# Kernel optimization log

Measured on AMD Instinct MI355X. Metric: run time of the kernel, lower is better.

## Reference

```python
import jax, jax.numpy as jnp
import numpy as np

B, N, M, DIM, H, DH = 2, 1024, 32, 128, 8, 16
DI = H * DH          # dim_inner = 128
S = 5                # sum of (1, max_degree, max_degree), max_degree = 2
DMLP = 256           # int(2.0 * dim_inner)
EPS = 1e-5
CLAMP = 50.0

def _ln(x, w):
    mu = x.mean(-1, keepdims=True)
    var = ((x - mu) ** 2).mean(-1, keepdims=True)
    return (x - mu) / jnp.sqrt(var + EPS) * w

def _split_heads(t):
    t = t.reshape(*t.shape[:-1], H, DH)
    return jnp.moveaxis(t, -2, 1)

def _gather(t, idx):
    # t: (b, h, n, ...), idx: (b, n, m) -> (b, h, n, m, ...)
    return jax.vmap(lambda tb, ib: tb[:, ib])(t, idx)

def setup_inputs():
    key = jax.random.key(0)
    ks = jax.random.split(key, 30)
    nrm = lambda i, shp, s=1.0: jax.random.normal(ks[i], shp, jnp.float32) * s
    return dict(
        h=nrm(0, (B, N, DIM)),
        t_ij=nrm(1, (B, N, M, DIM)),
        r_ij_1=nrm(2, (B, N, M, 3)),
        r_ij_2=nrm(3, (B, N, M, 5)),
        x_1=nrm(4, (B, N, DIM, 3)),
        x_2=nrm(5, (B, N, DIM, 5)),
        neighbor_indices=jax.random.randint(ks[6], (B, N, M), 0, N),
        neighbor_mask=jnp.ones((B, N, M), dtype=bool),
        ln_i_w=jnp.ones((DIM,)),
        ln_j_w=jnp.ones((DIM,)),
        Wq=nrm(7, (DIM, DI), DIM ** -0.5),
        Wk=nrm(8, (DIM, DI), DIM ** -0.5),
        Wv1=nrm(9, (DIM, DMLP), DIM ** -0.5), bv1=jnp.zeros((DMLP,)),
        Wv2=nrm(10, (DMLP, S * DI), DMLP ** -0.5), bv2=jnp.zeros((S * DI,)),
        Wpv1=nrm(11, (DIM, DMLP), DIM ** -0.5), bpv1=jnp.zeros((DMLP,)),
        Wpv2=nrm(12, (DMLP, S * DI), DMLP ** -0.5), bpv2=jnp.zeros((S * DI,)),
        Wek=nrm(13, (DIM, S * DI), DIM ** -0.5),
        Wev=nrm(14, (DIM, S * DI), DIM ** -0.5),
        Wg=nrm(15, (DIM, H * S), DIM ** -0.5), bg=jnp.zeros((H * S,)),
        Wo=nrm(16, (DI, DIM), DI ** -0.5),
    )

def reference(h, t_ij, r_ij_1, r_ij_2, x_1, x_2, neighbor_indices, neighbor_mask,
              ln_i_w, ln_j_w, Wq, Wk, Wv1, bv1, Wv2, bv2, Wpv1, bpv1, Wpv2, bpv2,
              Wek, Wev, Wg, bg, Wo):
    hi = _ln(h, ln_i_w)
    hj = _ln(h, ln_j_w)
    q = _split_heads(hi @ Wq)                                                   # (b,h,n,dh)
    k = _split_heads(hj @ Wk)                                                   # (b,h,n,dh)
    v = _split_heads((jax.nn.silu(hj @ Wv1 + bv1) @ Wv2 + bv2).reshape(B, N, S, DI))       # (b,h,n,s,dh)
    pv = _split_heads((jax.nn.silu(hj @ Wpv1 + bpv1) @ Wpv2 + bpv2).reshape(B, N, S, DI))  # (b,h,n,s,dh)
    ek = _split_heads(jax.nn.silu(t_ij @ Wek).reshape(B, N, M, S, DI))          # (b,h,i,j,s,dh)
    ev = _split_heads((t_ij @ Wev).reshape(B, N, M, S, DI))                     # (b,h,i,j,s,dh)

    idx = neighbor_indices
    k_n = _gather(k, idx)                                                        # (b,h,i,j,dh)
    v_n = _gather(v, idx)                                                        # (b,h,i,j,s,dh)
    pv_n = _gather(pv, idx)                                                      # (b,h,i,j,s,dh)

    keys = k_n[..., None, :] * ek                                                # (b,h,i,j,s,dh)
    sim = jnp.einsum('bhid,bhijsd->bhijs', q, keys)
    sim = jnp.tanh(sim / CLAMP) * CLAMP
    neg = -jnp.finfo(sim.dtype).max
    sim = jnp.where(neighbor_mask[:, None, :, :, None], sim, neg)
    attn = jax.nn.softmax(sim, axis=-2)                                          # softmax over neighbors j

    sea = attn[..., None] * v_n + ev * pv_n                                      # (b,h,i,j,s,dh)
    gates = jax.nn.sigmoid(hi @ Wg + bg).reshape(B, N, H, S)
    gates = jnp.moveaxis(gates, 2, 1)[:, :, :, None, :, None]                    # (b,h,i,1,s,1)
    out = sea * gates
    out = jnp.moveaxis(out, 1, -2).reshape(B, N, M, S, DI)                       # merge heads
    out = out @ Wo                                                               # (b,i,j,s,dim)

    h_res = out[:, :, :, 0, :].sum(axis=2)                                       # (b,i,dim)
    r_sc1, r_sc2 = out[:, :, :, 1, :], out[:, :, :, 2, :]
    x_sc1, x_sc2 = out[:, :, :, 3, :], out[:, :, :, 4, :]

    def deg_residual(r_ij_l, x_l, r_sc, x_sc):
        r_res = jnp.einsum('bijm,bijd->bidm', r_ij_l, r_sc)
        x_nbr = jax.vmap(lambda xb, ib: xb[ib])(x_l, idx)                        # (b,i,j,d,m)
        x_res = jnp.einsum('bijdm,bijd->bidm', x_nbr, x_sc)
        return r_res + x_res

    x_res_1 = deg_residual(r_ij_1, x_1, r_sc1, x_sc1)
    x_res_2 = deg_residual(r_ij_2, x_2, r_sc2, x_sc2)
    return (h_res, x_res_1, x_res_2)
```

## Files before the change

kernel.cpp:

```cpp
#include <hip/hip_runtime.h>
#include <hip/hip_bf16.h>
#include <math.h>

#define BB    2
#define NPTS  1024
#define MM    32
#define DIMM  128
#define HH    8
#define DHH   16
#define SS    5
#define DMLPC 256
#define SDI   640
#define NNODE (BB*NPTS)
#define NN128 (NNODE*DIMM)

typedef __attribute__((ext_vector_type(8))) short bf16x8;
typedef __attribute__((ext_vector_type(4))) float f32x4;
typedef __attribute__((ext_vector_type(4))) float fvec4;

__device__ __forceinline__ float frcp(float x){ return __builtin_amdgcn_rcpf(x); }
__device__ __forceinline__ float sigf(float x){ return frcp(1.0f+__expf(-x)); }
__device__ __forceinline__ float siluf(float x){ return x*frcp(1.0f+__expf(-x)); }
__device__ __forceinline__ unsigned short f2bf(float x){
  unsigned u = __float_as_uint(x);
  u += 0x7fffu + ((u>>16)&1u);
  return (unsigned short)(u>>16);
}
__device__ __forceinline__ float bfu2f(unsigned short u){ return __uint_as_float(((unsigned)u)<<16); }

#define SWZT 76544
#define T4C  2097152
__global__ __launch_bounds__(256) void prep_kernel(
    const float* __restrict__ Wq,  const float* __restrict__ Wk,
    const float* __restrict__ Wv1, const float* __restrict__ Wpv1,
    const float* __restrict__ Wv2, const float* __restrict__ Wpv2,
    const float* __restrict__ Wek, const float* __restrict__ Wev,
    const float* __restrict__ Wo,  const float* __restrict__ Wg,
    const float* __restrict__ t_ij, const float* __restrict__ x1g,
    const float* __restrict__ x2g,
    unsigned short* __restrict__ wsw, unsigned short* __restrict__ tb,
    unsigned short* __restrict__ x1p, unsigned short* __restrict__ x2p)
{
  int i = blockIdx.x*256 + threadIdx.x;
  if (i < SWZT){
    int f = i >> 6, lane = i & 63;
    const float* W; int ncols, nkt, fb;
    if      (f <   32){ W=Wq;   ncols=128; nkt=4; fb=0;    }
    else if (f <   64){ W=Wk;   ncols=128; nkt=4; fb=32;   }
    else if (f <  128){ W=Wv1;  ncols=256; nkt=4; fb=64;   }
    else if (f <  192){ W=Wpv1; ncols=256; nkt=4; fb=128;  }
    else if (f <  512){ W=Wv2;  ncols=640; nkt=8; fb=192;  }
    else if (f <  832){ W=Wpv2; ncols=640; nkt=8; fb=512;  }
    else if (f <  992){ W=Wek;  ncols=640; nkt=4; fb=832;  }
    else if (f < 1152){ W=Wev;  ncols=640; nkt=4; fb=992;  }
    else if (f < 1184){ W=Wo;   ncols=128; nkt=4; fb=1152; }
    else              { W=Wg;   ncols=40;  nkt=4; fb=1184; }
    int fl = f - fb;
    int kt = fl % nkt, nt = fl / nkt;
    int row = kt*32 + ((lane>>4)*8);
    int col = nt*16 + (lane&15);
    unsigned px[4];
    if (col < ncols){
      #pragma unroll
      for (int e2=0; e2<4; ++e2){
        unsigned lo = f2bf(W[(size_t)(row+2*e2  )*ncols + col]);
        unsigned hi = f2bf(W[(size_t)(row+2*e2+1)*ncols + col]);
        px[e2] = lo | (hi<<16);
      }
    } else {
      px[0]=px[1]=px[2]=px[3]=0u;
    }
    ((uint4*)wsw)[(size_t)f*64 + lane] = make_uint4(px[0],px[1],px[2],px[3]);
  } else if (i < SWZT + T4C){
    int q = i - SWZT;
    fvec4 v = __builtin_nontemporal_load((const fvec4*)t_ij + q);
    unsigned a = (unsigned)f2bf(v[0]) | ((unsigned)f2bf(v[1])<<16);
    unsigned b = (unsigned)f2bf(v[2]) | ((unsigned)f2bf(v[3])<<16);
    unsigned long long pv = (unsigned long long)a | ((unsigned long long)b << 32);
    __builtin_nontemporal_store(pv, (unsigned long long*)tb + q);
  } else if (i < SWZT + T4C + NN128){
    int nc = i - (SWZT + T4C);
    const float* sp = x1g + (size_t)nc*3;
    unsigned long long pk = (unsigned long long)f2bf(sp[0])
                          | ((unsigned long long)f2bf(sp[1])<<16)
                          | ((unsigned long long)f2bf(sp[2])<<32);
    __builtin_nontemporal_store(pk, (unsigned long long*)(x1p + (size_t)nc*4));
  } else {
    int nc = i - (SWZT + T4C + NN128);
    const float* sp = x2g + (size_t)nc*5;
    unsigned long long lo = (unsigned long long)f2bf(sp[0])
                          | ((unsigned long long)f2bf(sp[1])<<16)
                          | ((unsigned long long)f2bf(sp[2])<<32)
                          | ((unsigned long long)f2bf(sp[3])<<48);
    unsigned long long hi = (unsigned long long)f2bf(sp[4]);
    __builtin_nontemporal_store(lo, (unsigned long long*)(x2p + (size_t)nc*8));
    __builtin_nontemporal_store(hi, (unsigned long long*)(x2p + (size_t)nc*8 + 4));
  }
}

__global__ __launch_bounds__(256) void node_kernel(
    const float* __restrict__ h,
    const float* __restrict__ lniw, const float* __restrict__ lnjw,
    const unsigned short* __restrict__ wsw,
    const float* __restrict__ bv1, const float* __restrict__ bpv1,
    const float* __restrict__ bv2, const float* __restrict__ bpv2,
    const float* __restrict__ bg,
    unsigned short* __restrict__ qb, unsigned short* __restrict__ kb,
    unsigned short* __restrict__ vpvb, float* __restrict__ go)
{
  const int br  = blockIdx.x & 1;
  const int n0  = (blockIdx.x >> 1) * 16;
  const int tid = threadIdx.x;
  const int wid = tid>>6, lane = tid&63;
  const int u   = lane&15;

  const unsigned short* wqk_sw = wsw + (br ? 16384 : 0);
  const unsigned short* w1_sw  = wsw + (br ? 65536 : 32768);
  const unsigned short* w2_sw  = wsw + (br ? 262144 : 98304);
  const unsigned short* wg_sw  = wsw + 606208;
  const float* b1 = br ? bpv1 : bv1;
  const float* b2 = br ? bpv2 : bv2;

  __shared__ unsigned short hib[16][132], hjb[16][132];
  __shared__ unsigned short m1[16][260];

  {
    const int row = tid>>4, cg = tid&15;
    const float* hp = h + (size_t)(n0+row)*DIMM + cg*8;
    fvec4 p0 = *(const fvec4*)hp;
    fvec4 p1 = *(const fvec4*)(hp+4);
    float x[8] = {p0[0],p0[1],p0[2],p0[3],p1[0],p1[1],p1[2],p1[3]};
    float s1=0.f, s2=0.f;
    #pragma unroll
    for (int e=0;e<8;++e){ s1+=x[e]; s2+=x[e]*x[e]; }
    #pragma unroll
    for (int m=1;m<16;m<<=1){ s1+=__shfl_xor(s1,m); s2+=__shfl_xor(s2,m); }
    const float mu = s1*(1.f/DIMM), ms = s2*(1.f/DIMM);
    const float rstd = rsqrtf(ms-mu*mu+1e-5f);
    #pragma unroll
    for (int e=0;e<8;++e){
      float xn = (x[e]-mu)*rstd;
      int c = cg*8+e;
      hib[row][c] = f2bf(xn*lniw[c]);
      hjb[row][c] = f2bf(xn*lnjw[c]);
    }
  }
  __syncthreads();

  bf16x8 aj[4];
  #pragma unroll
  for (int kt=0;kt<4;++kt) aj[kt] = *(const bf16x8*)&hjb[u][kt*32+(lane>>4)*8];

  {
    bf16x8 afr[4];
    if (br == 0){
      #pragma unroll
      for (int kt=0;kt<4;++kt) afr[kt] = *(const bf16x8*)&hib[u][kt*32+(lane>>4)*8];
    } else {
      #pragma unroll
      for (int kt=0;kt<4;++kt) afr[kt] = aj[kt];
    }
    unsigned short* outb = br ? kb : qb;
    const bf16x8* bfp = (const bf16x8*)wqk_sw;
    for (int i2=0;i2<2;++i2){
      const int nt = wid*2+i2;
      f32x4 acc = {0.f,0.f,0.f,0.f};
      #pragma unroll
      for (int kt=0;kt<4;++kt)
        acc = __builtin_amdgcn_mfma_f32_16x16x32_bf16(afr[kt], bfp[(size_t)(nt*4+kt)*64+lane], acc, 0,0,0);
      #pragma unroll
      for (int r=0;r<4;++r)
        outb[(size_t)(n0+(lane>>4)*4+r)*DIMM + nt*16+u] = f2bf(acc[r]);
    }
  }

  {
    const bf16x8* bfp = (const bf16x8*)w1_sw;
    for (int i2=0;i2<4;++i2){
      const int nt = wid*4+i2;
      f32x4 acc = {0.f,0.f,0.f,0.f};
      #pragma unroll
      for (int kt=0;kt<4;++kt)
        acc = __builtin_amdgcn_mfma_f32_16x16x32_bf16(aj[kt], bfp[(size_t)(nt*4+kt)*64+lane], acc, 0,0,0);
      const float bv = b1[nt*16+u];
      #pragma unroll
      for (int r=0;r<4;++r)
        m1[(lane>>4)*4+r][nt*16+u] = f2bf(siluf(acc[r]+bv));
    }
  }
  __syncthreads();

  {
    bf16x8 am[8];
    #pragma unroll
    for (int kt=0;kt<8;++kt) am[kt] = *(const bf16x8*)&m1[u][kt*32+(lane>>4)*8];
    const bf16x8* bfp = (const bf16x8*)w2_sw;
    for (int i2=0;i2<10;++i2){
      const int nt = wid*10+i2;
      f32x4 acc = {0.f,0.f,0.f,0.f};
      #pragma unroll
      for (int kt=0;kt<8;++kt)
        acc = __builtin_amdgcn_mfma_f32_16x16x32_bf16(am[kt], bfp[(size_t)(nt*8+kt)*64+lane], acc, 0,0,0);
      const int c = nt*16+u, s = c>>7, d = c&127;
      const float bb = b2[c];
      #pragma unroll
      for (int r=0;r<4;++r)
        vpvb[(size_t)(n0+(lane>>4)*4+r)*(SS*256) + s*256 + d*2 + br] = f2bf(acc[r]+bb);
    }
  }

  if (br == 0 && wid == 0){
    bf16x8 ai[4];
    #pragma unroll
    for (int kt=0;kt<4;++kt) ai[kt] = *(const bf16x8*)&hib[u][kt*32+(lane>>4)*8];
    const bf16x8* bfp = (const bf16x8*)wg_sw;
    #pragma unroll
    for (int nt=0;nt<3;++nt){
      f32x4 acc = {0.f,0.f,0.f,0.f};
      #pragma unroll
      for (int kt=0;kt<4;++kt)
        acc = __builtin_amdgcn_mfma_f32_16x16x32_bf16(ai[kt], bfp[(size_t)(nt*4+kt)*64+lane], acc, 0,0,0);
      const int col = nt*16+u;
      if (col < HH*SS){
        const float bb = bg[col];
        #pragma unroll
        for (int r=0;r<4;++r)
          go[(size_t)(n0+(lane>>4)*4+r)*(HH*SS) + col] = sigf(acc[r]+bb);
      }
    }
  }
}

__global__ __launch_bounds__(256) void edge_kernel(
    const unsigned short* __restrict__ tb,
    const float* __restrict__ r1g, const float* __restrict__ r2g,
    const unsigned short* __restrict__ x1p, const unsigned short* __restrict__ x2p,
    const int*  __restrict__ nbr,
    const unsigned short* __restrict__ wsw,
    const unsigned short* __restrict__ qb, const unsigned short* __restrict__ kb,
    const unsigned short* __restrict__ vpvb,
    const float* __restrict__ go,
    float* __restrict__ out,
    float* __restrict__ p1, float* __restrict__ p2,
    float* __restrict__ p3, float* __restrict__ p4,
    int use_atomic)
{
  const int bid = blockIdx.x;
  const int xcd = bid & 7, wslot = bid >> 3;
  const int nid = xcd*256 + (wslot & 255);
  const int s   = wslot >> 8;
  const int b0  = nid >> 10;
  const int tid = threadIdx.x;
  const int wid = tid >> 6, lane = tid & 63;
  const int u   = lane & 15;
  const int g4  = (lane >> 4) * 4;

  const bf16x8* wekf = (const bf16x8*)(wsw + 425984);
  const bf16x8* wevf = (const bf16x8*)(wsw + 507904);
  const bf16x8* wof  = (const bf16x8*)(wsw + 589824);

  __shared__ unsigned short buf_lds[MM][132];
  __shared__ float          sim_s[HH][33];
  __shared__ float          g_s[HH];
  __shared__ float          r_s[MM][5];

  bf16x8 afr[2][4];
  {
    const unsigned short* tp = tb + (size_t)nid*MM*DIMM;
    #pragma unroll
    for (int mt=0; mt<2; ++mt)
      #pragma unroll
      for (int kt=0; kt<4; ++kt)
        afr[mt][kt] = *(const bf16x8*)&tp[(mt*16+u)*DIMM + kt*32 + g4*2];
  }

  #pragma unroll
  for (int it=0; it<4; ++it){
    int e = tid + it*256;
    int j = e>>5, d = (e&31)*4;
    int nj = nbr[nid*MM + j];
    *(uint2*)&buf_lds[j][d] = *(const uint2*)&kb[(unsigned)(b0*NPTS + nj)*DIMM + d];
  }
  int njr[2][4];
  #pragma unroll
  for (int mt=0; mt<2; ++mt)
    #pragma unroll
    for (int r=0; r<4; ++r)
      njr[mt][r] = nbr[nid*MM + mt*16 + g4 + r];
  if (tid < HH) g_s[tid] = go[nid*HH*SS + tid*SS + s];
  if (s == 1){ for (int e=tid; e<MM*3; e+=256) r_s[e/3][e%3] = r1g[(size_t)nid*MM*3 + e]; }
  if (s == 2){ for (int e=tid; e<MM*5; e+=256) r_s[e/5][e%5] = r2g[(size_t)nid*MM*5 + e]; }
  const float ql = bfu2f(qb[(unsigned)nid*DIMM + wid*16 + u]);
  const float qh = bfu2f(qb[(unsigned)nid*DIMM + (wid+4)*16 + u]);
  const unsigned* vpvu = (const unsigned*)vpvb;
  unsigned vp[2][2][4];
  #pragma unroll
  for (int hl=0; hl<2; ++hl){
    const int col = (wid*2+hl)*16 + u;
    #pragma unroll
    for (int mt=0; mt<2; ++mt)
      #pragma unroll
      for (int r=0; r<4; ++r)
        vp[hl][mt][r] = vpvu[(unsigned)(b0*NPTS + njr[mt][r])*(SS*DIMM) + s*DIMM + col];
  }
  __syncthreads();

  #pragma unroll
  for (int i=0; i<2; ++i){
    const int hh = wid + 4*i;
    const int nt = s*8 + hh;
    const float qv = i ? qh : ql;
    f32x4 acc0 = {0.f,0.f,0.f,0.f}, acc1 = {0.f,0.f,0.f,0.f};
    #pragma unroll
    for (int kt=0; kt<4; ++kt){
      bf16x8 bfr = wekf[(size_t)(nt*4+kt)*64 + lane];
      acc0 = __builtin_amdgcn_mfma_f32_16x16x32_bf16(afr[0][kt], bfr, acc0, 0,0,0);
      acc1 = __builtin_amdgcn_mfma_f32_16x16x32_bf16(afr[1][kt], bfr, acc1, 0,0,0);
    }
    #pragma unroll
    for (int mt=0; mt<2; ++mt){
      #pragma unroll
      for (int r=0; r<4; ++r){
        int j = mt*16 + g4 + r;
        float val = (mt==0) ? acc0[r] : acc1[r];
        float p = siluf(val) * qv * bfu2f(buf_lds[j][hh*16 + u]);
        p += __shfl_xor(p,1); p += __shfl_xor(p,2);
        p += __shfl_xor(p,4); p += __shfl_xor(p,8);
        if (u == 0) sim_s[hh][j] = p;
      }
    }
  }
  __syncthreads();

  {
    const int hh = tid >> 5, j = tid & 31;
    float praw = sim_s[hh][j];
    float v = 50.f - 100.f*frcp(__expf(praw*0.04f) + 1.f);
    float e = __expf(v);
    float sum = e;
    #pragma unroll
    for (int m=1; m<32; m<<=1) sum += __shfl_xor(sum,m);
    sim_s[hh][j] = g_s[hh] * e * frcp(sum);
  }
  __syncthreads();

  #pragma unroll
  for (int hl=0; hl<2; ++hl){
    const int hh = wid*2 + hl;
    const int nt = s*8 + hh;
    const int col = hh*16 + u;
    const float gp = g_s[hh];
    f32x4 acc0 = {0.f,0.f,0.f,0.f}, acc1 = {0.f,0.f,0.f,0.f};
    #pragma unroll
    for (int kt=0; kt<4; ++kt){
      bf16x8 bfr = wevf[(size_t)(nt*4+kt)*64 + lane];
      acc0 = __builtin_amdgcn_mfma_f32_16x16x32_bf16(afr[0][kt], bfr, acc0, 0,0,0);
      acc1 = __builtin_amdgcn_mfma_f32_16x16x32_bf16(afr[1][kt], bfr, acc1, 0,0,0);
    }
    #pragma unroll
    for (int mt=0; mt<2; ++mt){
      #pragma unroll
      for (int r=0; r<4; ++r){
        int j = mt*16 + g4 + r;
        float evv = (mt==0) ? acc0[r] : acc1[r];
        unsigned w = vp[hl][mt][r];
        float vn  = bfu2f((unsigned short)(w & 0xffffu));
        float pvn = bfu2f((unsigned short)(w >> 16));
        float sea = sim_s[hh][j]*vn + gp*evv*pvn;
        buf_lds[j][col] = f2bf(sea);
      }
    }
  }
  __syncthreads();

  float hres[2] = {0.f,0.f};
  float xr1[2][3] = {{0.f,0.f,0.f},{0.f,0.f,0.f}};
  float xr2[2][5] = {{0.f,0.f,0.f,0.f,0.f},{0.f,0.f,0.f,0.f,0.f}};
  #pragma unroll
  for (int ntl=0; ntl<2; ++ntl){
    const int col = (wid*2+ntl)*16 + u;
    #pragma unroll
    for (int mt=0; mt<2; ++mt){
      f32x4 acc = {0.f,0.f,0.f,0.f};
      #pragma unroll
      for (int kt=0; kt<4; ++kt){
        bf16x8 a = *(const bf16x8*)&buf_lds[mt*16 + u][kt*32 + g4*2];
        bf16x8 wfr = wof[(size_t)((wid*2+ntl)*4+kt)*64 + lane];
        acc = __builtin_amdgcn_mfma_f32_16x16x32_bf16(a, wfr, acc, 0,0,0);
      }
      #pragma unroll
      for (int r=0; r<4; ++r){
        int j = mt*16 + g4 + r;
        float ov = acc[r];
        if (s == 0){
          hres[ntl] += ov;
        } else if (s == 1){
          #pragma unroll
          for (int m=0;m<3;++m) xr1[ntl][m] += r_s[j][m]*ov;
        } else if (s == 2){
          #pragma unroll
          for (int m=0;m<5;++m) xr2[ntl][m] += r_s[j][m]*ov;
        } else if (s == 3){
          unsigned idx = (unsigned)(b0*NPTS + njr[mt][r])*DIMM + col;
          uint2 w2 = *(const uint2*)&x1p[(size_t)idx*4];
          xr1[ntl][0] += bfu2f((unsigned short)(w2.x & 0xffffu))*ov;
          xr1[ntl][1] += bfu2f((unsigned short)(w2.x >> 16))*ov;
          xr1[ntl][2] += bfu2f((unsigned short)(w2.y & 0xffffu))*ov;
        } else {
          unsigned idx = (unsigned)(b0*NPTS + njr[mt][r])*DIMM + col;
          uint4 w4 = *(const uint4*)&x2p[(size_t)idx*8];
          xr2[ntl][0] += bfu2f((unsigned short)(w4.x & 0xffffu))*ov;
          xr2[ntl][1] += bfu2f((unsigned short)(w4.x >> 16))*ov;
          xr2[ntl][2] += bfu2f((unsigned short)(w4.y & 0xffffu))*ov;
          xr2[ntl][3] += bfu2f((unsigned short)(w4.y >> 16))*ov;
          xr2[ntl][4] += bfu2f((unsigned short)(w4.z & 0xffffu))*ov;
        }
      }
    }
  }

  #pragma unroll
  for (int ntl=0; ntl<2; ++ntl){
    hres[ntl] += __shfl_xor(hres[ntl],16); hres[ntl] += __shfl_xor(hres[ntl],32);
    #pragma unroll
    for (int m=0;m<3;++m){ xr1[ntl][m] += __shfl_xor(xr1[ntl][m],16); xr1[ntl][m] += __shfl_xor(xr1[ntl][m],32); }
    #pragma unroll
    for (int m=0;m<5;++m){ xr2[ntl][m] += __shfl_xor(xr2[ntl][m],16); xr2[ntl][m] += __shfl_xor(xr2[ntl][m],32); }
  }
  if (lane < 16){
    const size_t b1 = (size_t)NNODE*DIMM;
    const size_t b2 = b1 + (size_t)NNODE*DIMM*3;
    #pragma unroll
    for (int ntl=0; ntl<2; ++ntl){
      int col = (wid*2+ntl)*16 + lane;
      size_t nc = (size_t)nid*DIMM + col;
      if (s == 0){
        __builtin_nontemporal_store(hres[ntl], &out[nc]);
      } else if (use_atomic){
        if (s == 1 || s == 3){
          #pragma unroll
          for (int m=0;m<3;++m) atomicAdd(&out[b1 + nc*3 + m], xr1[ntl][m]);
        } else {
          #pragma unroll
          for (int m=0;m<5;++m) atomicAdd(&out[b2 + nc*5 + m], xr2[ntl][m]);
        }
      } else {
        if (s == 1){      for (int m=0;m<3;++m) p1[nc*3+m] = xr1[ntl][m]; }
        else if (s == 2){ for (int m=0;m<5;++m) p2[nc*5+m] = xr2[ntl][m]; }
        else if (s == 3){ for (int m=0;m<3;++m) p3[nc*3+m] = xr1[ntl][m]; }
        else {            for (int m=0;m<5;++m) p4[nc*5+m] = xr2[ntl][m]; }
      }
    }
  }
}

__global__ __launch_bounds__(256) void combine_kernel(
    const float* __restrict__ p1, const float* __restrict__ p2,
    const float* __restrict__ p3, const float* __restrict__ p4,
    float* __restrict__ out)
{
  const int N1 = NNODE*DIMM*3/4;
  int i = blockIdx.x*256 + threadIdx.x;
  if (i < N1){
    fvec4 a = ((const fvec4*)p1)[i];
    fvec4 b = ((const fvec4*)p3)[i];
    ((fvec4*)(out + NNODE*DIMM))[i] = a + b;
  } else {
    int q = i - N1;
    fvec4 a = ((const fvec4*)p2)[q];
    fvec4 b = ((const fvec4*)p4)[q];
    ((fvec4*)(out + NNODE*DIMM*4))[q] = a + b;
  }
}

extern "C" void kernel_launch(void* const* d_in, const int* in_sizes, int n_in,
                              void* d_out, int out_size, void* d_ws, size_t ws_size,
                              hipStream_t stream) {
  const float* h    = (const float*)d_in[0];
  const float* t_ij = (const float*)d_in[1];
  const float* r1g  = (const float*)d_in[2];
  const float* r2g  = (const float*)d_in[3];
  const float* x1g  = (const float*)d_in[4];
  const float* x2g  = (const float*)d_in[5];
  const int*   nbr  = (const int*)d_in[6];
  const float* lniw = (const float*)d_in[8];
  const float* lnjw = (const float*)d_in[9];
  const float* Wq   = (const float*)d_in[10];
  const float* Wk   = (const float*)d_in[11];
  const float* Wv1  = (const float*)d_in[12];
  const float* bv1  = (const float*)d_in[13];
  const float* Wv2  = (const float*)d_in[14];
  const float* bv2  = (const float*)d_in[15];
  const float* Wpv1 = (const float*)d_in[16];
  const float* bpv1 = (const float*)d_in[17];
  const float* Wpv2 = (const float*)d_in[18];
  const float* bpv2 = (const float*)d_in[19];
  const float* Wek  = (const float*)d_in[20];
  const float* Wev  = (const float*)d_in[21];
  const float* Wg   = (const float*)d_in[22];
  const float* bg   = (const float*)d_in[23];
  const float* Wo   = (const float*)d_in[24];

  char* w = (char*)d_ws;
  #define CARVE(ty, name, count) ty* name = (ty*)w; w += (((size_t)(count))*sizeof(ty) + 255) & ~(size_t)255;
  CARVE(unsigned short, qb,   (size_t)NNODE*DIMM)
  CARVE(unsigned short, kb,   (size_t)NNODE*DIMM)
  CARVE(unsigned short, vpvb, (size_t)NNODE*SS*256)
  CARVE(float,          go,   (size_t)NNODE*HH*SS)
  CARVE(unsigned short, x1p,  (size_t)NN128*4)
  CARVE(unsigned short, x2p,  (size_t)NN128*8)
  CARVE(unsigned short, tb,   (size_t)NNODE*MM*DIMM)
  CARVE(unsigned short, wsw,  (size_t)1196*512)
  CARVE(float, p1, (size_t)NN128*3)
  CARVE(float, p2, (size_t)NN128*5)
  CARVE(float, p3, (size_t)NN128*3)
  CARVE(float, p4, (size_t)NN128*5)
  #undef CARVE
  int use_atomic = ((size_t)(w - (char*)d_ws) > ws_size) ? 1 : 0;

  float* outp = (float*)d_out;

  if (use_atomic){
    hipError_t _e = hipMemsetAsync(outp + (size_t)NNODE*DIMM, 0,
                                   (size_t)NNODE*DIMM*8*sizeof(float), stream);
    (void)_e;
  }

  prep_kernel<<<10539, 256, 0, stream>>>(Wq, Wk, Wv1, Wpv1, Wv2, Wpv2,
      Wek, Wev, Wo, Wg, t_ij, x1g, x2g, wsw, tb, x1p, x2p);

  node_kernel<<<NNODE/16*2, 256, 0, stream>>>(h, lniw, lnjw, wsw,
      bv1, bpv1, bv2, bpv2, bg, qb, kb, vpvb, go);

  edge_kernel<<<NNODE*SS, 256, 0, stream>>>(tb, r1g, r2g, x1p, x2p, nbr,
      wsw, qb, kb, vpvb, go, outp, p1, p2, p3, p4, use_atomic);

  if (!use_atomic){
    combine_kernel<<<2048, 256, 0, stream>>>(p1, p2, p3, p4, outp);
  }
}
```

Before: 179.2 us.

## Process all five output slots per node in one edge block and drop combine pass

The edge kernel now launches one block per node and loops over the five output slots internally. It used to launch a separate block per (node, slot). This lets the t_ij MFMA fragments, the gathered k rows, the neighbor indices, the gates and the r_ij values be loaded once and reused across slots. The next slot's v/pv gather is prefetched while the current slot's sea tile is written. Heads are remapped so that each wave owns its own rows of sim_s, which removes two block barriers per slot. Because every block now holds full per-node sums, it writes the outputs directly, and the partial buffers, atomic fallback and combine kernel are removed. The trade-off is a five times smaller grid with longer, more serial blocks, which gives fewer resident blocks to hide gather latency.

```diff
diff --git a/kernel.cpp b/kernel.cpp
--- a/kernel.cpp
+++ b/kernel.cpp
@@ -240,15 +240,10 @@
     const unsigned short* __restrict__ qb, const unsigned short* __restrict__ kb,
     const unsigned short* __restrict__ vpvb,
     const float* __restrict__ go,
-    float* __restrict__ out,
-    float* __restrict__ p1, float* __restrict__ p2,
-    float* __restrict__ p3, float* __restrict__ p4,
-    int use_atomic)
+    float* __restrict__ out)
 {
   const int bid = blockIdx.x;
-  const int xcd = bid & 7, wslot = bid >> 3;
-  const int nid = xcd*256 + (wslot & 255);
-  const int s   = wslot >> 8;
+  const int nid = ((bid & 7) << 8) | (bid >> 3);
   const int b0  = nid >> 10;
   const int tid = threadIdx.x;
   const int wid = tid >> 6, lane = tid & 63;
@@ -259,10 +254,12 @@
   const bf16x8* wevf = (const bf16x8*)(wsw + 507904);
   const bf16x8* wof  = (const bf16x8*)(wsw + 589824);
 
-  __shared__ unsigned short buf_lds[MM][132];
+  __shared__ unsigned short kn_lds[MM][132];
+  __shared__ unsigned short sea_lds[MM][132];
   __shared__ float          sim_s[HH][33];
-  __shared__ float          g_s[HH];
-  __shared__ float          r_s[MM][5];
+  __shared__ float          g_s[HH*SS];
+  __shared__ float          r1_s[MM][3];
+  __shared__ float          r2_s[MM][5];
 
   bf16x8 afr[2][4];
   {
@@ -273,13 +270,12 @@
       for (int kt=0; kt<4; ++kt)
         afr[mt][kt] = *(const bf16x8*)&tp[(mt*16+u)*DIMM + kt*32 + g4*2];
   }
-
   #pragma unroll
   for (int it=0; it<4; ++it){
     int e = tid + it*256;
     int j = e>>5, d = (e&31)*4;
     int nj = nbr[nid*MM + j];
-    *(uint2*)&buf_lds[j][d] = *(const uint2*)&kb[(unsigned)(b0*NPTS + nj)*DIMM + d];
+    *(uint2*)&kn_lds[j][d] = *(const uint2*)&kb[(unsigned)(b0*NPTS + nj)*DIMM + d];
   }
   int njr[2][4];
   #pragma unroll
@@ -287,11 +283,12 @@
     #pragma unroll
     for (int r=0; r<4; ++r)
       njr[mt][r] = nbr[nid*MM + mt*16 + g4 + r];
-  if (tid < HH) g_s[tid] = go[nid*HH*SS + tid*SS + s];
-  if (s == 1){ for (int e=tid; e<MM*3; e+=256) r_s[e/3][e%3] = r1g[(size_t)nid*MM*3 + e]; }
-  if (s == 2){ for (int e=tid; e<MM*5; e+=256) r_s[e/5][e%5] = r2g[(size_t)nid*MM*5 + e]; }
-  const float ql = bfu2f(qb[(unsigned)nid*DIMM + wid*16 + u]);
-  const float qh = bfu2f(qb[(unsigned)nid*DIMM + (wid+4)*16 + u]);
+  if (tid < HH*SS) g_s[tid] = go[nid*HH*SS + tid];
+  for (int e=tid; e<MM*3; e+=256) r1_s[e/3][e%3] = r1g[(size_t)nid*MM*3 + e];
+  for (int e=tid; e<MM*5; e+=256) r2_s[e/5][e%5] = r2g[(size_t)nid*MM*5 + e];
+  const float ql = bfu2f(qb[(unsigned)nid*DIMM + (wid*2  )*16 + u]);
+  const float qh = bfu2f(qb[(unsigned)nid*DIMM + (wid*2+1)*16 + u]);
+
   const unsigned* vpvu = (const unsigned*)vpvb;
   unsigned vp[2][2][4];
   #pragma unroll
@@ -301,122 +298,134 @@
     for (int mt=0; mt<2; ++mt)
       #pragma unroll
       for (int r=0; r<4; ++r)
-        vp[hl][mt][r] = vpvu[(unsigned)(b0*NPTS + njr[mt][r])*(SS*DIMM) + s*DIMM + col];
-  }
-  __syncthreads();
-
-  #pragma unroll
-  for (int i=0; i<2; ++i){
-    const int hh = wid + 4*i;
-    const int nt = s*8 + hh;
-    const float qv = i ? qh : ql;
-    f32x4 acc0 = {0.f,0.f,0.f,0.f}, acc1 = {0.f,0.f,0.f,0.f};
-    #pragma unroll
-    for (int kt=0; kt<4; ++kt){
-      bf16x8 bfr = wekf[(size_t)(nt*4+kt)*64 + lane];
-      acc0 = __builtin_amdgcn_mfma_f32_16x16x32_bf16(afr[0][kt], bfr, acc0, 0,0,0);
-      acc1 = __builtin_amdgcn_mfma_f32_16x16x32_bf16(afr[1][kt], bfr, acc1, 0,0,0);
-    }
-    #pragma unroll
-    for (int mt=0; mt<2; ++mt){
-      #pragma unroll
-      for (int r=0; r<4; ++r){
-        int j = mt*16 + g4 + r;
-        float val = (mt==0) ? acc0[r] : acc1[r];
-        float p = siluf(val) * qv * bfu2f(buf_lds[j][hh*16 + u]);
-        p += __shfl_xor(p,1); p += __shfl_xor(p,2);
-        p += __shfl_xor(p,4); p += __shfl_xor(p,8);
-        if (u == 0) sim_s[hh][j] = p;
-      }
-    }
-  }
-  __syncthreads();
-
-  {
-    const int hh = tid >> 5, j = tid & 31;
-    float praw = sim_s[hh][j];
-    float v = 50.f - 100.f*frcp(__expf(praw*0.04f) + 1.f);
-    float e = __expf(v);
-    float sum = e;
-    #pragma unroll
-    for (int m=1; m<32; m<<=1) sum += __shfl_xor(sum,m);
-    sim_s[hh][j] = g_s[hh] * e * frcp(sum);
-  }
-  __syncthreads();
-
-  #pragma unroll
-  for (int hl=0; hl<2; ++hl){
-    const int hh = wid*2 + hl;
-    const int nt = s*8 + hh;
-    const int col = hh*16 + u;
-    const float gp = g_s[hh];
-    f32x4 acc0 = {0.f,0.f,0.f,0.f}, acc1 = {0.f,0.f,0.f,0.f};
-    #pragma unroll
-    for (int kt=0; kt<4; ++kt){
-      bf16x8 bfr = wevf[(size_t)(nt*4+kt)*64 + lane];
-      acc0 = __builtin_amdgcn_mfma_f32_16x16x32_bf16(afr[0][kt], bfr, acc0, 0,0,0);
-      acc1 = __builtin_amdgcn_mfma_f32_16x16x32_bf16(afr[1][kt], bfr, acc1, 0,0,0);
-    }
-    #pragma unroll
-    for (int mt=0; mt<2; ++mt){
-      #pragma unroll
-      for (int r=0; r<4; ++r){
-        int j = mt*16 + g4 + r;
-        float evv = (mt==0) ? acc0[r] : acc1[r];
-        unsigned w = vp[hl][mt][r];
-        float vn  = bfu2f((unsigned short)(w & 0xffffu));
-        float pvn = bfu2f((unsigned short)(w >> 16));
-        float sea = sim_s[hh][j]*vn + gp*evv*pvn;
-        buf_lds[j][col] = f2bf(sea);
-      }
-    }
+        vp[hl][mt][r] = vpvu[(unsigned)(b0*NPTS + njr[mt][r])*(SS*DIMM) + 0*DIMM + col];
   }
   __syncthreads();
 
   float hres[2] = {0.f,0.f};
   float xr1[2][3] = {{0.f,0.f,0.f},{0.f,0.f,0.f}};
   float xr2[2][5] = {{0.f,0.f,0.f,0.f,0.f},{0.f,0.f,0.f,0.f,0.f}};
+
   #pragma unroll
-  for (int ntl=0; ntl<2; ++ntl){
-    const int col = (wid*2+ntl)*16 + u;
-    #pragma unroll
-    for (int mt=0; mt<2; ++mt){
-      f32x4 acc = {0.f,0.f,0.f,0.f};
+  for (int s=0; s<SS; ++s){
+    #pragma unroll
+    for (int hl=0; hl<2; ++hl){
+      const int hh = wid*2 + hl;
+      const int nt = s*8 + hh;
+      const float qv = hl ? qh : ql;
+      f32x4 acc0 = {0.f,0.f,0.f,0.f}, acc1 = {0.f,0.f,0.f,0.f};
       #pragma unroll
       for (int kt=0; kt<4; ++kt){
-        bf16x8 a = *(const bf16x8*)&buf_lds[mt*16 + u][kt*32 + g4*2];
-        bf16x8 wfr = wof[(size_t)((wid*2+ntl)*4+kt)*64 + lane];
-        acc = __builtin_amdgcn_mfma_f32_16x16x32_bf16(a, wfr, acc, 0,0,0);
-      }
-      #pragma unroll
-      for (int r=0; r<4; ++r){
-        int j = mt*16 + g4 + r;
-        float ov = acc[r];
-        if (s == 0){
-          hres[ntl] += ov;
-        } else if (s == 1){
+        bf16x8 bfr = wekf[(size_t)(nt*4+kt)*64 + lane];
+        acc0 = __builtin_amdgcn_mfma_f32_16x16x32_bf16(afr[0][kt], bfr, acc0, 0,0,0);
+        acc1 = __builtin_amdgcn_mfma_f32_16x16x32_bf16(afr[1][kt], bfr, acc1, 0,0,0);
+      }
+      #pragma unroll
+      for (int mt=0; mt<2; ++mt){
+        #pragma unroll
+        for (int r=0; r<4; ++r){
+          int j = mt*16 + g4 + r;
+          float val = (mt==0) ? acc0[r] : acc1[r];
+          float p = siluf(val) * qv * bfu2f(kn_lds[j][hh*16 + u]);
+          p += __shfl_xor(p,1); p += __shfl_xor(p,2);
+          p += __shfl_xor(p,4); p += __shfl_xor(p,8);
+          if (u == 0) sim_s[hh][j] = p;
+        }
+      }
+    }
+    {
+      const int hh = tid >> 5, j = tid & 31;
+      float praw = sim_s[hh][j];
+      float v = 50.f - 100.f*frcp(__expf(praw*0.04f) + 1.f);
+      float e = __expf(v);
+      float sum = e;
+      #pragma unroll
+      for (int m=1; m<32; m<<=1) sum += __shfl_xor(sum,m);
+      sim_s[hh][j] = g_s[hh*SS + s] * e * frcp(sum);
+    }
+    #pragma unroll
+    for (int hl=0; hl<2; ++hl){
+      const int hh = wid*2 + hl;
+      const int nt = s*8 + hh;
+      const int col = hh*16 + u;
+      const float gp = g_s[hh*SS + s];
+      f32x4 acc0 = {0.f,0.f,0.f,0.f}, acc1 = {0.f,0.f,0.f,0.f};
+      #pragma unroll
+      for (int kt=0; kt<4; ++kt){
+        bf16x8 bfr = wevf[(size_t)(nt*4+kt)*64 + lane];
+        acc0 = __builtin_amdgcn_mfma_f32_16x16x32_bf16(afr[0][kt], bfr, acc0, 0,0,0);
+        acc1 = __builtin_amdgcn_mfma_f32_16x16x32_bf16(afr[1][kt], bfr, acc1, 0,0,0);
+      }
+      #pragma unroll
+      for (int mt=0; mt<2; ++mt){
+        #pragma unroll
+        for (int r=0; r<4; ++r){
+          int j = mt*16 + g4 + r;
+          float evv = (mt==0) ? acc0[r] : acc1[r];
+          unsigned w = vp[hl][mt][r];
+          float vn  = bfu2f((unsigned short)(w & 0xffffu));
+          float pvn = bfu2f((unsigned short)(w >> 16));
+          float sea = sim_s[hh][j]*vn + gp*evv*pvn;
+          sea_lds[j][col] = f2bf(sea);
+        }
+      }
+    }
+    if (s < SS-1){
+      #pragma unroll
+      for (int hl=0; hl<2; ++hl){
+        const int col = (wid*2+hl)*16 + u;
+        #pragma unroll
+        for (int mt=0; mt<2; ++mt)
           #pragma unroll
-          for (int m=0;m<3;++m) xr1[ntl][m] += r_s[j][m]*ov;
-        } else if (s == 2){
-          #pragma unroll
-          for (int m=0;m<5;++m) xr2[ntl][m] += r_s[j][m]*ov;
-        } else if (s == 3){
-          unsigned idx = (unsigned)(b0*NPTS + njr[mt][r])*DIMM + col;
-          uint2 w2 = *(const uint2*)&x1p[(size_t)idx*4];
-          xr1[ntl][0] += bfu2f((unsigned short)(w2.x & 0xffffu))*ov;
-          xr1[ntl][1] += bfu2f((unsigned short)(w2.x >> 16))*ov;
-          xr1[ntl][2] += bfu2f((unsigned short)(w2.y & 0xffffu))*ov;
-        } else {
-          unsigned idx = (unsigned)(b0*NPTS + njr[mt][r])*DIMM + col;
-          uint4 w4 = *(const uint4*)&x2p[(size_t)idx*8];
-          xr2[ntl][0] += bfu2f((unsigned short)(w4.x & 0xffffu))*ov;
-          xr2[ntl][1] += bfu2f((unsigned short)(w4.x >> 16))*ov;
-          xr2[ntl][2] += bfu2f((unsigned short)(w4.y & 0xffffu))*ov;
-          xr2[ntl][3] += bfu2f((unsigned short)(w4.y >> 16))*ov;
-          xr2[ntl][4] += bfu2f((unsigned short)(w4.z & 0xffffu))*ov;
+          for (int r=0; r<4; ++r)
+            vp[hl][mt][r] = vpvu[(unsigned)(b0*NPTS + njr[mt][r])*(SS*DIMM) + (s+1)*DIMM + col];
+      }
+    }
+    __syncthreads();
+
+    #pragma unroll
+    for (int ntl=0; ntl<2; ++ntl){
+      const int col = (wid*2+ntl)*16 + u;
+      #pragma unroll
+      for (int mt=0; mt<2; ++mt){
+        f32x4 acc = {0.f,0.f,0.f,0.f};
+        #pragma unroll
+        for (int kt=0; kt<4; ++kt){
+          bf16x8 a = *(const bf16x8*)&sea_lds[mt*16 + u][kt*32 + g4*2];
+          bf16x8 wfr = wof[(size_t)((wid*2+ntl)*4+kt)*64 + lane];
+          acc = __builtin_amdgcn_mfma_f32_16x16x32_bf16(a, wfr, acc, 0,0,0);
         }
-      }
-    }
+        #pragma unroll
+        for (int r=0; r<4; ++r){
+          int j = mt*16 + g4 + r;
+          float ov = acc[r];
+          if (s == 0){
+            hres[ntl] += ov;
+          } else if (s == 1){
+            #pragma unroll
+            for (int m=0;m<3;++m) xr1[ntl][m] += r1_s[j][m]*ov;
+          } else if (s == 2){
+            #pragma unroll
+            for (int m=0;m<5;++m) xr2[ntl][m] += r2_s[j][m]*ov;
+          } else if (s == 3){
+            unsigned idx = (unsigned)(b0*NPTS + njr[mt][r])*DIMM + col;
+            uint2 w2 = *(const uint2*)&x1p[(size_t)idx*4];
+            xr1[ntl][0] += bfu2f((unsigned short)(w2.x & 0xffffu))*ov;
+            xr1[ntl][1] += bfu2f((unsigned short)(w2.x >> 16))*ov;
+            xr1[ntl][2] += bfu2f((unsigned short)(w2.y & 0xffffu))*ov;
+          } else {
+            unsigned idx = (unsigned)(b0*NPTS + njr[mt][r])*DIMM + col;
+            uint4 w4 = *(const uint4*)&x2p[(size_t)idx*8];
+            xr2[ntl][0] += bfu2f((unsigned short)(w4.x & 0xffffu))*ov;
+            xr2[ntl][1] += bfu2f((unsigned short)(w4.x >> 16))*ov;
+            xr2[ntl][2] += bfu2f((unsigned short)(w4.y & 0xffffu))*ov;
+            xr2[ntl][3] += bfu2f((unsigned short)(w4.y >> 16))*ov;
+            xr2[ntl][4] += bfu2f((unsigned short)(w4.z & 0xffffu))*ov;
+          }
+        }
+      }
+    }
+    __syncthreads();
   }
 
   #pragma unroll
@@ -434,42 +443,14 @@
     for (int ntl=0; ntl<2; ++ntl){
       int col = (wid*2+ntl)*16 + lane;
       size_t nc = (size_t)nid*DIMM + col;
-      if (s == 0){
-        __builtin_nontemporal_store(hres[ntl], &out[nc]);
-      } else if (use_atomic){
-        if (s == 1 || s == 3){
-          #pragma unroll
-          for (int m=0;m<3;++m) atomicAdd(&out[b1 + nc*3 + m], xr1[ntl][m]);
-        } else {
-          #pragma unroll
-          for (int m=0;m<5;++m) atomicAdd(&out[b2 + nc*5 + m], xr2[ntl][m]);
-        }
-      } else {
-        if (s == 1){      for (int m=0;m<3;++m) p1[nc*3+m] = xr1[ntl][m]; }
-        else if (s == 2){ for (int m=0;m<5;++m) p2[nc*5+m] = xr2[ntl][m]; }
-        else if (s == 3){ for (int m=0;m<3;++m) p3[nc*3+m] = xr1[ntl][m]; }
-        else {            for (int m=0;m<5;++m) p4[nc*5+m] = xr2[ntl][m]; }
-      }
-    }
-  }
-}
-
-__global__ __launch_bounds__(256) void combine_kernel(
-    const float* __restrict__ p1, const float* __restrict__ p2,
-    const float* __restrict__ p3, const float* __restrict__ p4,
-    float* __restrict__ out)
-{
-  const int N1 = NNODE*DIMM*3/4;
-  int i = blockIdx.x*256 + threadIdx.x;
-  if (i < N1){
-    fvec4 a = ((const fvec4*)p1)[i];
-    fvec4 b = ((const fvec4*)p3)[i];
-    ((fvec4*)(out + NNODE*DIMM))[i] = a + b;
-  } else {
-    int q = i - N1;
-    fvec4 a = ((const fvec4*)p2)[q];
-    fvec4 b = ((const fvec4*)p4)[q];
-    ((fvec4*)(out + NNODE*DIMM*4))[q] = a + b;
+      __builtin_nontemporal_store(hres[ntl], &out[nc]);
+      #pragma unroll
+      for (int m=0;m<3;++m)
+        __builtin_nontemporal_store(xr1[ntl][m], &out[b1 + nc*3 + m]);
+      #pragma unroll
+      for (int m=0;m<5;++m)
+        __builtin_nontemporal_store(xr2[ntl][m], &out[b2 + nc*5 + m]);
+    }
   }
 }
 
@@ -511,20 +492,9 @@
   CARVE(unsigned short, x2p,  (size_t)NN128*8)
   CARVE(unsigned short, tb,   (size_t)NNODE*MM*DIMM)
   CARVE(unsigned short, wsw,  (size_t)1196*512)
-  CARVE(float, p1, (size_t)NN128*3)
-  CARVE(float, p2, (size_t)NN128*5)
-  CARVE(float, p3, (size_t)NN128*3)
-  CARVE(float, p4, (size_t)NN128*5)
   #undef CARVE
-  int use_atomic = ((size_t)(w - (char*)d_ws) > ws_size) ? 1 : 0;
 
   float* outp = (float*)d_out;
-
-  if (use_atomic){
-    hipError_t _e = hipMemsetAsync(outp + (size_t)NNODE*DIMM, 0,
-                                   (size_t)NNODE*DIMM*8*sizeof(float), stream);
-    (void)_e;
-  }
 
   prep_kernel<<<10539, 256, 0, stream>>>(Wq, Wk, Wv1, Wpv1, Wv2, Wpv2,
       Wek, Wev, Wo, Wg, t_ij, x1g, x2g, wsw, tb, x1p, x2p);
@@ -532,10 +502,6 @@
   node_kernel<<<NNODE/16*2, 256, 0, stream>>>(h, lniw, lnjw, wsw,
       bv1, bpv1, bv2, bpv2, bg, qb, kb, vpvb, go);
 
-  edge_kernel<<<NNODE*SS, 256, 0, stream>>>(tb, r1g, r2g, x1p, x2p, nbr,
-      wsw, qb, kb, vpvb, go, outp, p1, p2, p3, p4, use_atomic);
-
-  if (!use_atomic){
-    combine_kernel<<<2048, 256, 0, stream>>>(p1, p2, p3, p4, outp);
-  }
+  edge_kernel<<<NNODE, 256, 0, stream>>>(tb, r1g, r2g, x1p, x2p, nbr,
+      wsw, qb, kb, vpvb, go, outp);
 }
```

Result: slower. 274.3 us (+53.1%).
